# Kernel optimization log

Measured on AMD Instinct MI355X. Metric: run time of the kernel, lower is better.

Reference implementation:

```python
import jax, jax.numpy as jnp
import numpy as np

H = 16      # num_heads
D = 64      # hidden_size per head
IN = 1024   # input_size = H*D
B, S = 4, 2048

def setup_inputs() -> dict:
    key = jax.random.key(0)
    ks = jax.random.split(key, 5)
    scale = 1.0 / np.sqrt(IN)
    return {
        "x": jax.random.normal(ks[0], (B, S, IN), dtype=jnp.float32),
        "Wq": jax.random.normal(ks[1], (IN, H * D), dtype=jnp.float32) * scale,
        "bq": jnp.zeros((H * D,), dtype=jnp.float32),
        "Wk": jax.random.normal(ks[2], (IN, H * D), dtype=jnp.float32) * scale,
        "bk": jnp.zeros((H * D,), dtype=jnp.float32),
        "Wv": jax.random.normal(ks[3], (IN, H * D), dtype=jnp.float32) * scale,
        "bv": jnp.zeros((H * D,), dtype=jnp.float32),
        "Wo": jax.random.normal(ks[4], (H * D, IN), dtype=jnp.float32) * scale,
        "bo": jnp.zeros((IN,), dtype=jnp.float32),
    }

def reference(x, Wq, bq, Wk, bk, Wv, bv, Wo, bo):
    b, s, _ = x.shape
    # projections -> [b, h, s, d]
    def split_heads(t):
        return t.reshape(b, s, H, D).transpose(0, 2, 1, 3)
    q = split_heads(x @ Wq + bq)
    k = split_heads(x @ Wk + bk)
    v = split_heads(x @ Wv + bv)
    scores = jnp.einsum('bhqd,bhkd->bhqk', q, k) / jnp.sqrt(jnp.float32(D))
    probs = jax.nn.softmax(scores, axis=-1)            # [b,h,s,s]
    attn = jnp.einsum('bhqk,bhkd->bhqd', probs, v)     # [b,h,s,d]
    attn = attn.transpose(0, 2, 1, 3).reshape(b, s, H * D)
    out = attn @ Wo + bo
    return out, jnp.mean(probs, axis=1)
```

## Files before the change

kernel.cpp:

```cpp
#include <hip/hip_runtime.h>

typedef __attribute__((ext_vector_type(8))) short s8v;
typedef __attribute__((ext_vector_type(4))) short s4v;
typedef __attribute__((ext_vector_type(4))) float f4v;

#define DEV __device__ __forceinline__

DEV short b16(float f) {
  unsigned u = __builtin_bit_cast(unsigned, f);
  u = (u + 0x7fffu + ((u >> 16) & 1u)) >> 16;
  return (short)u;
}

DEV unsigned pk2(float a, float b) {
#if __has_builtin(__builtin_amdgcn_cvt_pk_bf16_f32)
  auto p = __builtin_amdgcn_cvt_pk_bf16_f32(a, b);
  return __builtin_bit_cast(unsigned, p);
#else
  return (unsigned)(unsigned short)b16(a) | ((unsigned)(unsigned short)b16(b) << 16);
#endif
}

DEV float fexp2(float x) {
#if __has_builtin(__builtin_amdgcn_exp2f)
  return __builtin_amdgcn_exp2f(x);
#else
  return exp2f(x);
#endif
}

DEV void gl_lds16(const short* g, short* l) {
  __builtin_amdgcn_global_load_lds((const __attribute__((address_space(1))) void*)g,
                                   (__attribute__((address_space(3))) void*)l, 16, 0, 0);
}

#define WAIT_VM(N) asm volatile("s_waitcnt vmcnt(" #N ")" ::: "memory")
#define WAIT_LGKM0() asm volatile("s_waitcnt lgkmcnt(0)" ::: "memory")
#define BAR() __builtin_amdgcn_s_barrier()
#define PRIO1() __builtin_amdgcn_s_setprio(1)
#define PRIO0() __builtin_amdgcn_s_setprio(0)

__global__ __launch_bounds__(256) void prep(const float* __restrict__ x, short* __restrict__ xb,
                                            const float* __restrict__ W0, const float* __restrict__ W1,
                                            const float* __restrict__ W2, const float* __restrict__ W3,
                                            short* __restrict__ Wt) {
  const int tid = threadIdx.x;
  if (blockIdx.x < 8192) {
    int i = blockIdx.x * 256 + tid;
    float4 v = ((const float4*)x)[i];
    s4v o; o.x = b16(v.x); o.y = b16(v.y); o.z = b16(v.z); o.w = b16(v.w);
    ((s4v*)xb)[i] = o;
  } else {
    int wid = blockIdx.x - 8192;
    const int mat = wid >> 9;
    const float* W = mat == 0 ? W0 : (mat == 1 ? W1 : (mat == 2 ? W2 : W3));
    short* out = Wt + (long)mat * 1048576;
    int id = (wid & 511) * 256 + tid;
    int k8 = id >> 10;
    int n  = id & 1023;
    s8v o;
#pragma unroll
    for (int j = 0; j < 8; ++j) o[j] = b16(W[(k8 * 8 + j) * 1024 + n]);
    *(s8v*)&out[n * 1024 + k8 * 8] = o;
  }
}

__global__ __launch_bounds__(256) void gemm_qkv(const short* __restrict__ A,
                                                const short* __restrict__ Wt,
                                                const float* __restrict__ bq,
                                                const float* __restrict__ bk,
                                                const float* __restrict__ bv,
                                                short* __restrict__ Cb,
                                                short* __restrict__ Vt, float qscale) {
  __shared__ short AB[32768];
  int n = blockIdx.x + 24 * blockIdx.y;
  int id = (n & 7) * 192 + (n >> 3);
  const int nx = id % 24, my = id / 24;
  const int mat = nx >> 3;
  const short* Bt = Wt + (long)mat * 1048576;
  const float* bias = mat == 0 ? bq : (mat == 1 ? bk : bv);
  short* Cout = Cb + (long)mat * 8388608;
  const float scale = mat == 0 ? qscale : 1.0f;
  const int m0 = my * 128, n0 = (nx & 7) * 128;
  const int tid = threadIdx.x;
  const int w = tid >> 6, lane = tid & 63, quad = lane >> 4, l15 = lane & 15;
  const int wm = w >> 1, wn = w & 1;
  const int lr = lane >> 3, lc = (lane & 7) * 8;
  f4v acc[4][4] = {};
#pragma unroll
  for (int i = 0; i < 4; ++i) {
    int c = i * 4 + w;
    int r = c * 8 + lr;
    gl_lds16(&A[(m0 + r) * 1024 + lc], &AB[c * 512]);
    gl_lds16(&Bt[(n0 + r) * 1024 + lc], &AB[8192 + c * 512]);
  }
  for (int t = 0; t < 16; ++t) {
    const int cur = (t & 1) * 16384;
    WAIT_VM(0);
    WAIT_LGKM0();
    BAR();
    if (t < 15) {
      const int nxt = ((t + 1) & 1) * 16384;
      const int k0 = (t + 1) * 64;
#pragma unroll
      for (int i = 0; i < 4; ++i) {
        int c = i * 4 + w;
        int r = c * 8 + lr;
        gl_lds16(&A[(m0 + r) * 1024 + k0 + lc], &AB[nxt + c * 512]);
        gl_lds16(&Bt[(n0 + r) * 1024 + k0 + lc], &AB[nxt + 8192 + c * 512]);
      }
    }
    const short* As = &AB[cur];
    const short* Bs = &AB[cur + 8192];
#pragma unroll
    for (int kk = 0; kk < 2; ++kk) {
      s8v af[4], bf[4];
#pragma unroll
      for (int mt = 0; mt < 4; ++mt) af[mt] = *(const s8v*)&As[(wm * 64 + mt * 16 + l15) * 64 + kk * 32 + quad * 8];
#pragma unroll
      for (int nt = 0; nt < 4; ++nt) bf[nt] = *(const s8v*)&Bs[(wn * 64 + nt * 16 + l15) * 64 + kk * 32 + quad * 8];
#pragma unroll
      for (int mt = 0; mt < 4; ++mt)
#pragma unroll
        for (int nt = 0; nt < 4; ++nt)
          acc[mt][nt] = __builtin_amdgcn_mfma_f32_16x16x32_bf16(af[mt], bf[nt], acc[mt][nt], 0, 0, 0);
    }
  }
  if (mat == 2) {
    __syncthreads();
    short* T = AB;
#pragma unroll
    for (int nt = 0; nt < 4; ++nt) {
      const int c = wn * 64 + nt * 16 + l15;
      const float bcol = bias[n0 + c];
#pragma unroll
      for (int mt = 0; mt < 4; ++mt) {
        const int sr = wm * 64 + mt * 16 + quad * 4;
#pragma unroll
        for (int r = 0; r < 4; ++r) {
          int s = sr + r;
          T[c * 128 + ((((s >> 3) ^ (c & 15))) << 3) + (s & 7)] = b16(acc[mt][nt][r] + bcol);
        }
      }
    }
    __syncthreads();
    const int b = m0 >> 11, s0 = m0 & 2047, h0 = n0 >> 6;
#pragma unroll
    for (int i = 0; i < 8; ++i) {
      int unit = tid + i * 256;
      int c = unit >> 4, s8 = unit & 15;
      s8v v = *(const s8v*)&T[c * 128 + ((s8 ^ (c & 15)) << 3)];
      *(s8v*)&Vt[(((long)(b * 16 + h0 + (c >> 6)) * 64) + (c & 63)) * 2048 + s0 + s8 * 8] = v;
    }
  } else {
#pragma unroll
    for (int nt = 0; nt < 4; ++nt) {
      const int col = n0 + wn * 64 + nt * 16 + l15;
      const float bcol = bias[col];
#pragma unroll
      for (int mt = 0; mt < 4; ++mt)
#pragma unroll
        for (int r = 0; r < 4; ++r) {
          const int row = m0 + wm * 64 + mt * 16 + quad * 4 + r;
          Cout[row * 1024 + col] = b16((acc[mt][nt][r] + bcol) * scale);
        }
    }
  }
}

__global__ __launch_bounds__(256) void gemm128(const short* __restrict__ A,
                                               const short* __restrict__ Bt,
                                               const float* __restrict__ bias,
                                               float* __restrict__ Cout) {
  __shared__ short AB[32768];
  int n = blockIdx.x + 8 * blockIdx.y;
  int id = (n & 7) * 64 + (n >> 3);
  const int m0 = (id >> 3) * 128, n0 = (id & 7) * 128;
  const int tid = threadIdx.x;
  const int w = tid >> 6, lane = tid & 63, quad = lane >> 4, l15 = lane & 15;
  const int wm = w >> 1, wn = w & 1;
  const int lr = lane >> 3, lc = (lane & 7) * 8;
  f4v acc[4][4] = {};
#pragma unroll
  for (int i = 0; i < 4; ++i) {
    int c = i * 4 + w;
    int r = c * 8 + lr;
    gl_lds16(&A[(m0 + r) * 1024 + lc], &AB[c * 512]);
    gl_lds16(&Bt[(n0 + r) * 1024 + lc], &AB[8192 + c * 512]);
  }
  for (int t = 0; t < 16; ++t) {
    const int cur = (t & 1) * 16384;
    WAIT_VM(0);
    WAIT_LGKM0();
    BAR();
    if (t < 15) {
      const int nxt = ((t + 1) & 1) * 16384;
      const int k0 = (t + 1) * 64;
#pragma unroll
      for (int i = 0; i < 4; ++i) {
        int c = i * 4 + w;
        int r = c * 8 + lr;
        gl_lds16(&A[(m0 + r) * 1024 + k0 + lc], &AB[nxt + c * 512]);
        gl_lds16(&Bt[(n0 + r) * 1024 + k0 + lc], &AB[nxt + 8192 + c * 512]);
      }
    }
    const short* As = &AB[cur];
    const short* Bs = &AB[cur + 8192];
#pragma unroll
    for (int kk = 0; kk < 2; ++kk) {
      s8v af[4], bf[4];
#pragma unroll
      for (int mt = 0; mt < 4; ++mt) af[mt] = *(const s8v*)&As[(wm * 64 + mt * 16 + l15) * 64 + kk * 32 + quad * 8];
#pragma unroll
      for (int nt = 0; nt < 4; ++nt) bf[nt] = *(const s8v*)&Bs[(wn * 64 + nt * 16 + l15) * 64 + kk * 32 + quad * 8];
#pragma unroll
      for (int mt = 0; mt < 4; ++mt)
#pragma unroll
        for (int nt = 0; nt < 4; ++nt)
          acc[mt][nt] = __builtin_amdgcn_mfma_f32_16x16x32_bf16(af[mt], bf[nt], acc[mt][nt], 0, 0, 0);
    }
  }
#pragma unroll
  for (int nt = 0; nt < 4; ++nt) {
    const int col = n0 + wn * 64 + nt * 16 + l15;
    const float bcol = bias[col];
#pragma unroll
    for (int mt = 0; mt < 4; ++mt)
#pragma unroll
      for (int r = 0; r < 4; ++r) {
        const int row = m0 + wm * 64 + mt * 16 + quad * 4 + r;
        Cout[row * 1024 + col] = acc[mt][nt][r] + bcol;
      }
  }
}

__global__ __launch_bounds__(256, 3) void attn_ctx(const short* __restrict__ Q, const short* __restrict__ K,
                                                   const short* __restrict__ Vt,
                                                   float* __restrict__ rbuf, short* __restrict__ ctx) {
  __shared__ __align__(16) char smem[49152];
  short* Ks = (short*)smem;
  short* Vs = (short*)(smem + 16384);
  short* Ps = (short*)(smem + 32768);
  short* Qs = Ps;
  int nlin = blockIdx.x + 32 * (blockIdx.y + 16 * blockIdx.z);
  int bid = (nlin & 7) * 256 + (nlin >> 3);
  const int q64 = bid & 31, h = (bid >> 5) & 15, b = bid >> 9;
  const int tid = threadIdx.x, w = tid >> 6, lane = tid & 63, quad = lane >> 4, l15 = lane & 15;
  const int bh = b * 16 + h, q0 = q64 * 64;

#pragma unroll
  for (int i = 0; i < 2; ++i) {
    int c = tid + i * 256;
    int r = c >> 3, cc = c & 7;
    *(s8v*)&Qs[r * 64 + (((cc ^ (r & 7))) << 3)] =
        *(const s8v*)&Q[((b * 2048 + q0 + r) * 16 + h) * 64 + cc * 8];
  }
  __syncthreads();
  s8v qf[4][2];
#pragma unroll
  for (int nt = 0; nt < 4; ++nt) {
    int r = nt * 16 + l15;
    qf[nt][0] = *(const s8v*)&Qs[r * 64 + ((quad ^ (r & 7)) << 3)];
    qf[nt][1] = *(const s8v*)&Qs[r * 64 + (((4 + quad) ^ (r & 7)) << 3)];
  }
  const short* kbase = &K[((long)(b * 2048) * 16 + h) * 64];
  const short* vbase = &Vt[(long)(bh * 64) * 2048];
  const int krow = w * 8 + (lane >> 3);
  const short* ksrc = kbase + krow * 1024 + (((lane & 7) ^ (lane >> 3)) << 3);
  const int vrow = w * 4 + (lane >> 4);
  const short* vsrc = vbase + vrow * 2048 + (((lane & 15) ^ vrow) << 3);
  f4v o[4] = {};
  f4v lf = {};
  s8v ones;
#pragma unroll
  for (int j = 0; j < 8; ++j) ones[j] = (short)0x3F80;

#pragma unroll
  for (int i = 0; i < 4; ++i) gl_lds16(ksrc + i * 32768, &Ks[(i * 4 + w) * 512]);
#pragma unroll
  for (int i = 0; i < 4; ++i) gl_lds16(vsrc + i * 32768, &Vs[(i * 4 + w) * 512]);
  WAIT_LGKM0();

  for (int kt = 0; kt < 16; ++kt) {
    WAIT_VM(4);
    BAR();
#pragma unroll
    for (int mt = 0; mt < 2; ++mt) {
      int kr = w * 32 + mt * 16 + l15;
      s8v a0 = *(const s8v*)&Ks[kr * 64 + ((quad ^ (kr & 7)) << 3)];
      s8v a1 = *(const s8v*)&Ks[kr * 64 + (((4 + quad) ^ (kr & 7)) << 3)];
#pragma unroll
      for (int nt = 0; nt < 4; ++nt) {
        f4v st = {};
        PRIO1();
        st = __builtin_amdgcn_mfma_f32_16x16x32_bf16(a0, qf[nt][0], st, 0, 0, 0);
        st = __builtin_amdgcn_mfma_f32_16x16x32_bf16(a1, qf[nt][1], st, 0, 0, 0);
        PRIO0();
        float e0 = fexp2(st[0]), e1 = fexp2(st[1]);
        float e2 = fexp2(st[2]), e3 = fexp2(st[3]);
        uint2 pp; pp.x = pk2(e0, e1); pp.y = pk2(e2, e3);
        int q = nt * 16 + l15;
        int chunk = (w * 4 + mt * 2 + (quad >> 1)) ^ l15;
        *(uint2*)&Ps[q * 128 + (chunk << 3) + (quad & 1) * 4] = pp;
      }
    }
    WAIT_LGKM0();
    BAR();
    if (kt < 15) {
#pragma unroll
      for (int i = 0; i < 4; ++i) gl_lds16(ksrc + (kt + 1) * 131072 + i * 32768, &Ks[(i * 4 + w) * 512]);
      WAIT_VM(4);
    } else {
      WAIT_VM(0);
    }
    BAR();
    PRIO1();
#pragma unroll
    for (int kk = 0; kk < 4; ++kk) {
      int qr = w * 16 + l15;
      s8v a = *(const s8v*)&Ps[qr * 128 + (((kk * 4 + quad) ^ (qr & 15)) << 3)];
#pragma unroll
      for (int dt = 0; dt < 4; ++dt) {
        int d = dt * 16 + l15;
        s8v vb = *(const s8v*)&Vs[d * 128 + (((kk * 4 + quad) ^ (d & 15)) << 3)];
        o[dt] = __builtin_amdgcn_mfma_f32_16x16x32_bf16(a, vb, o[dt], 0, 0, 0);
      }
      lf = __builtin_amdgcn_mfma_f32_16x16x32_bf16(a, ones, lf, 0, 0, 0);
    }
    PRIO0();
    WAIT_LGKM0();
    BAR();
    if (kt < 15) {
#pragma unroll
      for (int i = 0; i < 4; ++i) gl_lds16(vsrc + (kt + 1) * 128 + i * 32768, &Vs[(i * 4 + w) * 512]);
    }
  }

  float rv[4];
#pragma unroll
  for (int r = 0; r < 4; ++r) rv[r] = 1.0f / lf[r];
  if (l15 == 0) {
    f4v t; t[0] = rv[0]; t[1] = rv[1]; t[2] = rv[2]; t[3] = rv[3];
    *(f4v*)&rbuf[bh * 2048 + q0 + w * 16 + quad * 4] = t;
  }
#pragma unroll
  for (int dt = 0; dt < 4; ++dt)
#pragma unroll
    for (int r = 0; r < 4; ++r) {
      int sq = q0 + w * 16 + quad * 4 + r;
      ctx[((b * 2048 + sq) * 16 + h) * 64 + dt * 16 + l15] = b16(o[dt][r] * rv[r]);
    }
}

__global__ __launch_bounds__(256) void mean_probs(const short* __restrict__ Q, const short* __restrict__ K,
                                                  const float* __restrict__ rbuf, float* __restrict__ outm) {
  __shared__ __align__(16) short Qs[2][8192];
  __shared__ __align__(16) short Ks[2][8192];
  __shared__ __align__(16) float r_all[2048];
  int nlin = blockIdx.x + 16 * (blockIdx.y + 16 * blockIdx.z);
  int bid = (nlin & 7) * 128 + (nlin >> 3);
  const int k128 = bid & 15, q128 = (bid >> 4) & 15, b = bid >> 8;
  const int tid = threadIdx.x, w = tid >> 6, lane = tid & 63, quad = lane >> 4, l15 = lane & 15;
  f4v mn[2][8] = {};
  const int mrow = w * 8 + (lane >> 3);
  const int mck8 = ((lane & 7) ^ (lane >> 3)) << 3;
  const short* qsrc = Q + ((long)(b * 2048 + q128 * 128 + mrow) * 16) * 64 + mck8;
  const short* ksrc = K + ((long)(b * 2048 + k128 * 128 + mrow) * 16) * 64 + mck8;
  const float* rb = rbuf + (long)(b * 16) * 2048 + q128 * 128;
#pragma unroll
  for (int i = 0; i < 2; ++i) {
    int hh = i * 8 + w * 2 + (lane >> 5);
    gl_lds16((const short*)(rb + hh * 2048 + (lane & 31) * 4), (short*)r_all + (i * 4 + w) * 512);
  }
#pragma unroll
  for (int i = 0; i < 4; ++i) gl_lds16(qsrc + i * 32768, &Qs[0][(i * 4 + w) * 512]);
#pragma unroll
  for (int i = 0; i < 4; ++i) gl_lds16(ksrc + i * 32768, &Ks[0][(i * 4 + w) * 512]);

  for (int h = 0; h < 16; ++h) {
    const int cur = h & 1;
    WAIT_VM(0);
    BAR();
    if (h < 15) {
#pragma unroll
      for (int i = 0; i < 4; ++i) gl_lds16(qsrc + (h + 1) * 64 + i * 32768, &Qs[cur ^ 1][(i * 4 + w) * 512]);
#pragma unroll
      for (int i = 0; i < 4; ++i) gl_lds16(ksrc + (h + 1) * 64 + i * 32768, &Ks[cur ^ 1][(i * 4 + w) * 512]);
    }
    s8v aq[2][2];
#pragma unroll
    for (int qt = 0; qt < 2; ++qt) {
      int r = w * 32 + qt * 16 + l15;
      aq[qt][0] = *(const s8v*)&Qs[cur][r * 64 + ((quad ^ (r & 7)) << 3)];
      aq[qt][1] = *(const s8v*)&Qs[cur][r * 64 + (((4 + quad) ^ (r & 7)) << 3)];
    }
    float rr[2][4];
#pragma unroll
    for (int qt = 0; qt < 2; ++qt)
#pragma unroll
      for (int r = 0; r < 4; ++r) rr[qt][r] = r_all[h * 128 + w * 32 + qt * 16 + quad * 4 + r];
#pragma unroll
    for (int ktile = 0; ktile < 8; ++ktile) {
      int kr = ktile * 16 + l15;
      s8v b0 = *(const s8v*)&Ks[cur][kr * 64 + ((quad ^ (kr & 7)) << 3)];
      s8v b1 = *(const s8v*)&Ks[cur][kr * 64 + (((4 + quad) ^ (kr & 7)) << 3)];
#pragma unroll
      for (int qt = 0; qt < 2; ++qt) {
        f4v sc = {};
        sc = __builtin_amdgcn_mfma_f32_16x16x32_bf16(aq[qt][0], b0, sc, 0, 0, 0);
        sc = __builtin_amdgcn_mfma_f32_16x16x32_bf16(aq[qt][1], b1, sc, 0, 0, 0);
#pragma unroll
        for (int r = 0; r < 4; ++r)
          mn[qt][ktile][r] += fexp2(sc[r]) * rr[qt][r];
      }
    }
  }
#pragma unroll
  for (int qt = 0; qt < 2; ++qt)
#pragma unroll
    for (int ktile = 0; ktile < 8; ++ktile)
#pragma unroll
      for (int r = 0; r < 4; ++r) {
        long qrow = q128 * 128 + w * 32 + qt * 16 + quad * 4 + r;
        outm[((long)b * 2048 + qrow) * 2048 + k128 * 128 + ktile * 16 + l15] = mn[qt][ktile][r] * 0.0625f;
      }
}

extern "C" void kernel_launch(void* const* d_in, const int* in_sizes, int n_in,
                              void* d_out, int out_size, void* d_ws, size_t ws_size,
                              hipStream_t stream) {
  (void)in_sizes; (void)n_in; (void)out_size; (void)ws_size;
  const float* x  = (const float*)d_in[0];
  const float* Wq = (const float*)d_in[1];
  const float* bq = (const float*)d_in[2];
  const float* Wk = (const float*)d_in[3];
  const float* bk = (const float*)d_in[4];
  const float* Wv = (const float*)d_in[5];
  const float* bv = (const float*)d_in[6];
  const float* Wo = (const float*)d_in[7];
  const float* bo = (const float*)d_in[8];
  float* out  = (float*)d_out;
  float* outm = out + 8388608;

  char* ws = (char*)d_ws;
  short* xb  = (short*)(ws);
  short* Wqt = (short*)(ws + 16777216);
  short* Wot = (short*)(ws + 23068672);
  short* Qb  = (short*)(ws + 25165824);
  short* Kb  = (short*)(ws + 41943040);
  short* Vt  = (short*)(ws + 75497472);
  float* rbuf = (float*)(ws + 58720256);
  short* ctx = xb;

  const float C2 = 0.18033688011112042f;

  prep<<<10240, 256, 0, stream>>>(x, xb, Wq, Wk, Wv, Wo, Wqt);
  gemm_qkv<<<dim3(24, 64), 256, 0, stream>>>(xb, Wqt, bq, bk, bv, Qb, Vt, C2);
  attn_ctx<<<dim3(32, 16, 4), 256, 0, stream>>>(Qb, Kb, Vt, rbuf, ctx);
  mean_probs<<<dim3(16, 16, 4), 256, 0, stream>>>(Qb, Kb, rbuf, outm);
  gemm128<<<dim3(8, 64), 256, 0, stream>>>(ctx, Wot, bo, out);
}
```

Before: 400.5 us.

## Double-buffer K/V tiles and give each wave its own query rows in attention

The attention-context kernel now double-buffers the K and V tiles in LDS and issues the next tile's async loads at the start of each iteration. This removes the mid-loop load and wait phases and cuts the four barriers per iteration to one. Work is also repartitioned so each wave owns 16 query rows and computes scores across all 128 keys, which keeps its P tile private and needs no cross-wave sync between QK and PV. In exchange LDS use grows to 80KB and occupancy drops from 3 to 2 blocks per CU, and the s_setprio hints are removed.

After: 421.3 us. 5.2% more time.

```diff
diff --git a/kernel.cpp b/kernel.cpp
--- a/kernel.cpp
+++ b/kernel.cpp
@@ -37,8 +37,7 @@
 #define WAIT_VM(N) asm volatile("s_waitcnt vmcnt(" #N ")" ::: "memory")
 #define WAIT_LGKM0() asm volatile("s_waitcnt lgkmcnt(0)" ::: "memory")
 #define BAR() __builtin_amdgcn_s_barrier()
-#define PRIO1() __builtin_amdgcn_s_setprio(1)
-#define PRIO0() __builtin_amdgcn_s_setprio(0)
+#define SBAR() __builtin_amdgcn_sched_barrier(0)
 
 __global__ __launch_bounds__(256) void prep(const float* __restrict__ x, short* __restrict__ xb,
                                             const float* __restrict__ W0, const float* __restrict__ W1,
@@ -234,13 +233,11 @@
   }
 }
 
-__global__ __launch_bounds__(256, 3) void attn_ctx(const short* __restrict__ Q, const short* __restrict__ K,
+__global__ __launch_bounds__(256, 2) void attn_ctx(const short* __restrict__ Q, const short* __restrict__ K,
                                                    const short* __restrict__ Vt,
                                                    float* __restrict__ rbuf, short* __restrict__ ctx) {
-  __shared__ __align__(16) char smem[49152];
-  short* Ks = (short*)smem;
-  short* Vs = (short*)(smem + 16384);
-  short* Ps = (short*)(smem + 32768);
+  __shared__ __align__(16) char smem[81920];
+  short* Ps = (short*)(smem + 65536);
   short* Qs = Ps;
   int nlin = blockIdx.x + 32 * (blockIdx.y + 16 * blockIdx.z);
   int bid = (nlin & 7) * 256 + (nlin >> 3);
@@ -248,91 +245,78 @@
   const int tid = threadIdx.x, w = tid >> 6, lane = tid & 63, quad = lane >> 4, l15 = lane & 15;
   const int bh = b * 16 + h, q0 = q64 * 64;
 
-#pragma unroll
-  for (int i = 0; i < 2; ++i) {
-    int c = tid + i * 256;
-    int r = c >> 3, cc = c & 7;
-    *(s8v*)&Qs[r * 64 + (((cc ^ (r & 7))) << 3)] =
-        *(const s8v*)&Q[((b * 2048 + q0 + r) * 16 + h) * 64 + cc * 8];
-  }
-  __syncthreads();
-  s8v qf[4][2];
-#pragma unroll
-  for (int nt = 0; nt < 4; ++nt) {
-    int r = nt * 16 + l15;
-    qf[nt][0] = *(const s8v*)&Qs[r * 64 + ((quad ^ (r & 7)) << 3)];
-    qf[nt][1] = *(const s8v*)&Qs[r * 64 + (((4 + quad) ^ (r & 7)) << 3)];
-  }
   const short* kbase = &K[((long)(b * 2048) * 16 + h) * 64];
   const short* vbase = &Vt[(long)(bh * 64) * 2048];
   const int krow = w * 8 + (lane >> 3);
   const short* ksrc = kbase + krow * 1024 + (((lane & 7) ^ (lane >> 3)) << 3);
   const int vrow = w * 4 + (lane >> 4);
   const short* vsrc = vbase + vrow * 2048 + (((lane & 15) ^ vrow) << 3);
+
+#pragma unroll
+  for (int i = 0; i < 4; ++i) gl_lds16(ksrc + i * 32768, (short*)smem + (i * 4 + w) * 512);
+#pragma unroll
+  for (int i = 0; i < 4; ++i) gl_lds16(vsrc + i * 32768, (short*)(smem + 32768) + (i * 4 + w) * 512);
+
+#pragma unroll
+  for (int i = 0; i < 2; ++i) {
+    int c = tid + i * 256;
+    int r = c >> 3, cc = c & 7;
+    *(s8v*)&Qs[r * 64 + (((cc ^ (r & 7))) << 3)] =
+        *(const s8v*)&Q[((b * 2048 + q0 + r) * 16 + h) * 64 + cc * 8];
+  }
+  __syncthreads();
+  const int qrow = w * 16 + l15;
+  s8v qb0 = *(const s8v*)&Qs[qrow * 64 + ((quad ^ (qrow & 7)) << 3)];
+  s8v qb1 = *(const s8v*)&Qs[qrow * 64 + (((4 + quad) ^ (qrow & 7)) << 3)];
+  WAIT_LGKM0(); SBAR();
+
   f4v o[4] = {};
   f4v lf = {};
   s8v ones;
 #pragma unroll
   for (int j = 0; j < 8; ++j) ones[j] = (short)0x3F80;
 
-#pragma unroll
-  for (int i = 0; i < 4; ++i) gl_lds16(ksrc + i * 32768, &Ks[(i * 4 + w) * 512]);
-#pragma unroll
-  for (int i = 0; i < 4; ++i) gl_lds16(vsrc + i * 32768, &Vs[(i * 4 + w) * 512]);
-  WAIT_LGKM0();
-
   for (int kt = 0; kt < 16; ++kt) {
-    WAIT_VM(4);
-    BAR();
-#pragma unroll
-    for (int mt = 0; mt < 2; ++mt) {
-      int kr = w * 32 + mt * 16 + l15;
-      s8v a0 = *(const s8v*)&Ks[kr * 64 + ((quad ^ (kr & 7)) << 3)];
-      s8v a1 = *(const s8v*)&Ks[kr * 64 + (((4 + quad) ^ (kr & 7)) << 3)];
-#pragma unroll
-      for (int nt = 0; nt < 4; ++nt) {
-        f4v st = {};
-        PRIO1();
-        st = __builtin_amdgcn_mfma_f32_16x16x32_bf16(a0, qf[nt][0], st, 0, 0, 0);
-        st = __builtin_amdgcn_mfma_f32_16x16x32_bf16(a1, qf[nt][1], st, 0, 0, 0);
-        PRIO0();
-        float e0 = fexp2(st[0]), e1 = fexp2(st[1]);
-        float e2 = fexp2(st[2]), e3 = fexp2(st[3]);
-        uint2 pp; pp.x = pk2(e0, e1); pp.y = pk2(e2, e3);
-        int q = nt * 16 + l15;
-        int chunk = (w * 4 + mt * 2 + (quad >> 1)) ^ l15;
-        *(uint2*)&Ps[q * 128 + (chunk << 3) + (quad & 1) * 4] = pp;
-      }
-    }
+    const int cur = (kt & 1) * 16384;
+    const short* KsC = (const short*)(smem + cur);
+    const short* VsC = (const short*)(smem + 32768 + cur);
+    WAIT_VM(0);
     WAIT_LGKM0();
     BAR();
     if (kt < 15) {
-#pragma unroll
-      for (int i = 0; i < 4; ++i) gl_lds16(ksrc + (kt + 1) * 131072 + i * 32768, &Ks[(i * 4 + w) * 512]);
-      WAIT_VM(4);
-    } else {
-      WAIT_VM(0);
-    }
-    BAR();
-    PRIO1();
+      const int nxt = ((kt + 1) & 1) * 16384;
+#pragma unroll
+      for (int i = 0; i < 4; ++i)
+        gl_lds16(ksrc + (kt + 1) * 131072 + i * 32768, (short*)(smem + nxt) + (i * 4 + w) * 512);
+#pragma unroll
+      for (int i = 0; i < 4; ++i)
+        gl_lds16(vsrc + (kt + 1) * 128 + i * 32768, (short*)(smem + 32768 + nxt) + (i * 4 + w) * 512);
+    }
+#pragma unroll
+    for (int ktile = 0; ktile < 8; ++ktile) {
+      int kr = ktile * 16 + l15;
+      s8v a0 = *(const s8v*)&KsC[kr * 64 + ((quad ^ (kr & 7)) << 3)];
+      s8v a1 = *(const s8v*)&KsC[kr * 64 + (((4 + quad) ^ (kr & 7)) << 3)];
+      f4v st = {};
+      st = __builtin_amdgcn_mfma_f32_16x16x32_bf16(a0, qb0, st, 0, 0, 0);
+      st = __builtin_amdgcn_mfma_f32_16x16x32_bf16(a1, qb1, st, 0, 0, 0);
+      float e0 = fexp2(st[0]), e1 = fexp2(st[1]);
+      float e2 = fexp2(st[2]), e3 = fexp2(st[3]);
+      uint2 pp; pp.x = pk2(e0, e1); pp.y = pk2(e2, e3);
+      int chunk = (ktile * 2 + (quad >> 1)) ^ l15;
+      *(uint2*)&Ps[qrow * 128 + (chunk << 3) + (quad & 1) * 4] = pp;
+    }
+    WAIT_LGKM0(); SBAR();
 #pragma unroll
     for (int kk = 0; kk < 4; ++kk) {
-      int qr = w * 16 + l15;
-      s8v a = *(const s8v*)&Ps[qr * 128 + (((kk * 4 + quad) ^ (qr & 15)) << 3)];
+      s8v a = *(const s8v*)&Ps[qrow * 128 + (((kk * 4 + quad) ^ l15) << 3)];
 #pragma unroll
       for (int dt = 0; dt < 4; ++dt) {
         int d = dt * 16 + l15;
-        s8v vb = *(const s8v*)&Vs[d * 128 + (((kk * 4 + quad) ^ (d & 15)) << 3)];
+        s8v vb = *(const s8v*)&VsC[d * 128 + (((kk * 4 + quad) ^ (d & 15)) << 3)];
         o[dt] = __builtin_amdgcn_mfma_f32_16x16x32_bf16(a, vb, o[dt], 0, 0, 0);
       }
       lf = __builtin_amdgcn_mfma_f32_16x16x32_bf16(a, ones, lf, 0, 0, 0);
-    }
-    PRIO0();
-    WAIT_LGKM0();
-    BAR();
-    if (kt < 15) {
-#pragma unroll
-      for (int i = 0; i < 4; ++i) gl_lds16(vsrc + (kt + 1) * 128 + i * 32768, &Vs[(i * 4 + w) * 512]);
     }
   }
 
```
